# Kernel optimization log

Hardware: AMD Instinct MI355X
Metric: run time of the kernel (lower is better)

The kernel has to match this reference:

```python
import jax, jax.numpy as jnp
import numpy as np

N_NODES = 100000
D = 128
N_EDGES = 800000


def setup_inputs() -> dict:
    key = jax.random.key(0)
    k_feat, k_src, k_dst, k_ws, k_wn = jax.random.split(key, 5)
    scale = 1.0 / np.sqrt(D)
    return {
        "features": jax.random.normal(k_feat, (N_NODES, D), jnp.float32),
        "src": jax.random.randint(k_src, (N_EDGES,), 0, N_NODES, jnp.int32),
        "dst": jax.random.randint(k_dst, (N_EDGES,), 0, N_NODES, jnp.int32),
        "gamma": jnp.ones((D,), jnp.float32),
        "beta": jnp.zeros((D,), jnp.float32),
        "W_self": jax.random.normal(k_ws, (D, D), jnp.float32) * scale,
        "W_neigh": jax.random.normal(k_wn, (D, D), jnp.float32) * scale,
        "b": jnp.zeros((D,), jnp.float32),
    }


def reference(features, src, dst, gamma, beta, W_self, W_neigh, b):
    n = features.shape[0]
    eps = 1e-5
    # BatchNorm1d (training mode: batch stats over the node dim, biased var)
    mean = jnp.mean(features, axis=0)
    var = jnp.mean(jnp.square(features - mean), axis=0)
    h = (features - mean) * jax.lax.rsqrt(var + eps) * gamma + beta  # [N, D]

    # SAGEConv 'mean': gather source feats along edges, mean-reduce per dst node
    msg = h[src]  # [E, D] irregular gather
    agg = jax.ops.segment_sum(msg, dst, num_segments=n)  # [N, D]
    deg = jax.ops.segment_sum(jnp.ones(src.shape, h.dtype), dst, num_segments=n)
    h_neigh = agg / jnp.maximum(deg, 1.0)[:, None]  # zero-degree nodes stay 0

    conv = h @ W_self + h_neigh @ W_neigh + b  # fc_self + fc_neigh + bias
    out = conv + h  # skip connection
    return jax.nn.gelu(out, approximate=False)
```

## Files before the change

kernel.cpp:

```cpp
#include <hip/hip_runtime.h>

#define DD 128
#define NPB_LOG 8
#define NPB 256
#define EPB 2048

typedef __attribute__((ext_vector_type(8))) short short8;
typedef __attribute__((ext_vector_type(4))) float f32x4;
typedef __attribute__((ext_vector_type(2))) float f32x2;

__device__ inline unsigned short f2bf(float f) {
    unsigned u = __float_as_uint(f);
    unsigned r = u + 0x7fffu + ((u >> 16) & 1u);
    return (unsigned short)(r >> 16);
}

__global__ __launch_bounds__(256) void phase1_k(
    const float4* __restrict__ x, float* __restrict__ stats16, int n,
    const int* __restrict__ dst, int nE, int NCHUNK, int NBUCK,
    const float* __restrict__ Wself, const float* __restrict__ Wneigh,
    unsigned short* __restrict__ Bpre, int* __restrict__ cm) {
    int b = blockIdx.x, tid = threadIdx.x;
    __shared__ float ls[8][256];
    if (b < NCHUNK) {
        int chunk = b;
        int* cnt = (int*)ls;
        for (int i = tid; i < NBUCK; i += 256) cnt[i] = 0;
        __syncthreads();
        int e0 = chunk * EPB;
#pragma unroll
        for (int j = 0; j < 8; ++j) {
            int e = e0 + j * 256 + tid;
            if (e < nE) atomicAdd(&cnt[dst[e] >> NPB_LOG], 1);
        }
        __syncthreads();
        for (int bk = tid; bk < NBUCK; bk += 256)
            cm[(size_t)bk * NCHUNK + chunk] = cnt[bk];
    } else if (b < NCHUNK + 16) {
        int q = (b - NCHUNK) * 256 + tid;
        int l = q & 63;
        int kb = ((q >> 9) << 5) + ((l >> 4) << 3);
        int nn = (((q >> 6) & 7) << 4) + (l & 15);
        bool self = (kb < 128);
        const float* Wp = self ? (Wself + (size_t)kb * 128 + nn)
                               : (Wneigh + (size_t)(kb - 128) * 128 + nn);
        unsigned tmp[4];
#pragma unroll
        for (int j = 0; j < 4; ++j) {
            float v0 = Wp[(2 * j) * 128];
            float v1 = Wp[(2 * j + 1) * 128];
            if (self) {
                if (kb + 2 * j == nn) v0 += 1.0f;
                if (kb + 2 * j + 1 == nn) v1 += 1.0f;
            }
            tmp[j] = (unsigned)f2bf(v0) | ((unsigned)f2bf(v1) << 16);
        }
        uint4 w; w.x = tmp[0]; w.y = tmp[1]; w.z = tmp[2]; w.w = tmp[3];
        *(uint4*)(Bpre + (size_t)q * 8) = w;
    } else {
        int bb = b - NCHUNK - 16;
        int c4 = tid & 31, sub = tid >> 5;
        float sx = 0.f, sy = 0.f, sz = 0.f, sw = 0.f;
        float qx = 0.f, qy = 0.f, qz = 0.f, qw = 0.f;
        for (int r = bb * 8 + sub; r < n; r += 1024 * 8) {
            float4 v = x[(size_t)r * 32 + c4];
            sx += v.x; sy += v.y; sz += v.z; sw += v.w;
            qx += v.x * v.x; qy += v.y * v.y; qz += v.z * v.z; qw += v.w * v.w;
        }
        ls[sub][c4 * 4 + 0] = sx; ls[sub][c4 * 4 + 1] = sy;
        ls[sub][c4 * 4 + 2] = sz; ls[sub][c4 * 4 + 3] = sw;
        ls[sub][128 + c4 * 4 + 0] = qx; ls[sub][128 + c4 * 4 + 1] = qy;
        ls[sub][128 + c4 * 4 + 2] = qz; ls[sub][128 + c4 * 4 + 3] = qw;
        __syncthreads();
        float t = 0.f;
#pragma unroll
        for (int k = 0; k < 8; ++k) t += ls[k][tid];
        atomicAdd(&stats16[(bb & 15) * 256 + tid], t);
    }
}

__global__ __launch_bounds__(256) void scanA_k(
    const int* __restrict__ v_in, int* __restrict__ bsum, int n) {
    int b = blockIdx.x, t = threadIdx.x;
    int i0 = b * 1024 + t * 4;
    int4 v = {0, 0, 0, 0};
    if (i0 + 3 < n) v = *(const int4*)(v_in + i0);
    else {
        if (i0 < n) v.x = v_in[i0];
        if (i0 + 1 < n) v.y = v_in[i0 + 1];
        if (i0 + 2 < n) v.z = v_in[i0 + 2];
    }
    __shared__ int ls[256];
    ls[t] = v.x + v.y + v.z + v.w;
    __syncthreads();
#pragma unroll
    for (int off = 128; off > 0; off >>= 1) {
        if (t < off) ls[t] += ls[t + off];
        __syncthreads();
    }
    if (t == 0) bsum[b] = ls[0];
}

__global__ __launch_bounds__(256) void scanB_k(
    const int* __restrict__ bsum, int* __restrict__ bpref,
    int* __restrict__ total_out, int nb, int n,
    const float* __restrict__ stats16, const float* __restrict__ gamma,
    const float* __restrict__ beta, float* __restrict__ scsh, float inv_n) {
    int t = threadIdx.x;
    if (t < 128) {
        float s = 0.f, q = 0.f;
#pragma unroll
        for (int sh = 0; sh < 16; ++sh) {
            s += stats16[sh * 256 + t];
            q += stats16[sh * 256 + 128 + t];
        }
        float mean = s * inv_n;
        float var = q * inv_n - mean * mean;
        float sc = rsqrtf(var + 1e-5f) * gamma[t];
        scsh[t] = sc;
        scsh[128 + t] = beta[t] - mean * sc;
    }
    __shared__ int ls[256];
    ls[t] = (t < nb) ? bsum[t] : 0;
    __syncthreads();
#pragma unroll
    for (int off = 1; off < 256; off <<= 1) {
        int x = (t >= off) ? ls[t - off] : 0;
        __syncthreads();
        ls[t] += x;
        __syncthreads();
    }
    if (t < nb) bpref[t] = (t == 0) ? 0 : ls[t - 1];
    if (t == nb - 1) total_out[n] = ls[t];
}

__global__ __launch_bounds__(256) void scanC_k(
    const int* __restrict__ v_in, const int* __restrict__ bpref,
    int* __restrict__ o1, int* __restrict__ o2, int n) {
    int b = blockIdx.x, t = threadIdx.x;
    int i0 = b * 1024 + t * 4;
    int4 v = {0, 0, 0, 0};
    if (i0 + 3 < n) v = *(const int4*)(v_in + i0);
    else {
        if (i0 < n) v.x = v_in[i0];
        if (i0 + 1 < n) v.y = v_in[i0 + 1];
        if (i0 + 2 < n) v.z = v_in[i0 + 2];
    }
    int s = v.x + v.y + v.z + v.w;
    __shared__ int ls[256];
    ls[t] = s;
    __syncthreads();
#pragma unroll
    for (int off = 1; off < 256; off <<= 1) {
        int x = (t >= off) ? ls[t - off] : 0;
        __syncthreads();
        ls[t] += x;
        __syncthreads();
    }
    int run = bpref[b] + ((t == 0) ? 0 : ls[t - 1]);
    int4 o;
    o.x = run; o.y = run + v.x; o.z = o.y + v.y; o.w = o.z + v.z;
    if (i0 + 3 < n) {
        *(int4*)(o1 + i0) = o;
        *(int4*)(o2 + i0) = o;
    } else {
        if (i0 < n) { o1[i0] = o.x; o2[i0] = o.x; }
        if (i0 + 1 < n) { o1[i0 + 1] = o.y; o2[i0 + 1] = o.y; }
        if (i0 + 2 < n) { o1[i0 + 2] = o.z; o2[i0 + 2] = o.z; }
    }
}

__global__ __launch_bounds__(256) void phase2_k(
    const float4* __restrict__ x, const float* __restrict__ scsh,
    uint2* __restrict__ hbuf, unsigned* __restrict__ h8, int n,
    const int* __restrict__ src, const int* __restrict__ dst,
    const int* __restrict__ cmscan, unsigned* __restrict__ pairs,
    int nE, int NCHUNK, int NBUCK) {
    int b = blockIdx.x, tid = threadIdx.x;
    __shared__ int a[512];
    __shared__ int lcur[512];
    __shared__ int bas[512];
    __shared__ unsigned lsorted[EPB];
    __shared__ unsigned short lbk[EPB];
    if (b < NCHUNK) {
        int chunk = b;
        int e0 = chunk * EPB;
        int nv = min(EPB, nE - e0);
        for (int i = tid; i < 512; i += 256) a[i] = 0;
        __syncthreads();
        int myd[8];
#pragma unroll
        for (int j = 0; j < 8; ++j) {
            int e = e0 + j * 256 + tid;
            int d = (e < nE) ? dst[e] : -1;
            myd[j] = d;
            if (d >= 0) atomicAdd(&a[d >> NPB_LOG], 1);
        }
        for (int bk = tid; bk < NBUCK; bk += 256)
            bas[bk] = cmscan[(size_t)bk * NCHUNK + chunk];
        __syncthreads();
        for (int d = 1; d < 512; d <<= 1) {
            int idx = (tid + 1) * (d << 1) - 1;
            if (idx < 512) a[idx] += a[idx - d];
            __syncthreads();
        }
        if (tid == 0) a[511] = 0;
        __syncthreads();
        for (int d = 256; d >= 1; d >>= 1) {
            int idx = (tid + 1) * (d << 1) - 1;
            if (idx < 512) { int tm = a[idx - d]; a[idx - d] = a[idx]; a[idx] += tm; }
            __syncthreads();
        }
        for (int i = tid; i < 512; i += 256) lcur[i] = a[i];
        __syncthreads();
#pragma unroll
        for (int j = 0; j < 8; ++j) {
            int d = myd[j];
            if (d >= 0) {
                int e = e0 + j * 256 + tid;
                int bk = d >> NPB_LOG;
                int lp = atomicAdd(&lcur[bk], 1);
                lsorted[lp] = ((unsigned)src[e] << NPB_LOG) | (unsigned)(d & (NPB - 1));
                lbk[lp] = (unsigned short)bk;
            }
        }
        __syncthreads();
        for (int i = tid; i < nv; i += 256) {
            int bk = lbk[i];
            pairs[bas[bk] + i - a[bk]] = lsorted[i];
        }
    } else {
        int blk = b - NCHUNK;
        int c4 = tid & 31, sub = tid >> 5;
        int r0 = blk * 16 + sub, r1 = r0 + 8;
        float4 sc = ((const float4*)scsh)[c4];
        float4 sh = ((const float4*)(scsh + 128))[c4];
        bool ok0 = r0 < n, ok1 = r1 < n;
        float4 v0, v1;
        if (ok0) v0 = x[(size_t)r0 * 32 + c4];
        if (ok1) v1 = x[(size_t)r1 * 32 + c4];
        if (ok0) {
            float hx = v0.x * sc.x + sh.x, hy = v0.y * sc.y + sh.y;
            float hz = v0.z * sc.z + sh.z, hw = v0.w * sc.w + sh.w;
            uint2 o;
            o.x = (unsigned)f2bf(hx) | ((unsigned)f2bf(hy) << 16);
            o.y = (unsigned)f2bf(hz) | ((unsigned)f2bf(hw) << 16);
            hbuf[(size_t)r0 * 32 + c4] = o;
            int p8 = __builtin_amdgcn_cvt_pk_fp8_f32(hx, hy, 0, false);
            p8 = __builtin_amdgcn_cvt_pk_fp8_f32(hz, hw, p8, true);
            h8[(size_t)r0 * 32 + c4] = (unsigned)p8;
        }
        if (ok1) {
            float hx = v1.x * sc.x + sh.x, hy = v1.y * sc.y + sh.y;
            float hz = v1.z * sc.z + sh.z, hw = v1.w * sc.w + sh.w;
            uint2 o;
            o.x = (unsigned)f2bf(hx) | ((unsigned)f2bf(hy) << 16);
            o.y = (unsigned)f2bf(hz) | ((unsigned)f2bf(hw) << 16);
            hbuf[(size_t)r1 * 32 + c4] = o;
            int p8 = __builtin_amdgcn_cvt_pk_fp8_f32(hx, hy, 0, false);
            p8 = __builtin_amdgcn_cvt_pk_fp8_f32(hz, hw, p8, true);
            h8[(size_t)r1 * 32 + c4] = (unsigned)p8;
        }
    }
}

__global__ __launch_bounds__(256) void sortC_k(
    const unsigned* __restrict__ pairs, const int* __restrict__ cmscan,
    int* __restrict__ offsets, int* __restrict__ csr,
    int n, int nE, int NCHUNK, int NBUCK) {
    int b = blockIdx.x, tid = threadIdx.x;
    int base0 = cmscan[(size_t)b * NCHUNK];
    int end = (b + 1 < NBUCK) ? cmscan[(size_t)(b + 1) * NCHUNK] : nE;
    __shared__ int cnt[NPB];
    __shared__ int cur[NPB];
    cnt[tid] = 0;
    __syncthreads();
    for (int e = base0 + tid; e < end; e += 256)
        atomicAdd(&cnt[pairs[e] & (NPB - 1)], 1);
    __syncthreads();
    int c0 = cnt[tid];
    __shared__ int ps[256];
    ps[tid] = c0;
    __syncthreads();
#pragma unroll
    for (int off = 1; off < 256; off <<= 1) {
        int v = (tid >= off) ? ps[tid - off] : 0;
        __syncthreads();
        ps[tid] += v;
        __syncthreads();
    }
    int ex = base0 + ps[tid] - c0;
    cur[tid] = ex;
    int node = b * NPB + tid;
    if (node < n) offsets[node] = ex;
    if (b == NBUCK - 1 && tid == 0) offsets[n] = nE;
    __syncthreads();
    for (int e = base0 + tid; e < end; e += 256) {
        unsigned u = pairs[e];
        int p = atomicAdd(&cur[u & (NPB - 1)], 1);
        csr[p] = (int)(u >> NPB_LOG);
    }
}

#define ACC8(v)                                                       \
    do {                                                              \
        acc[0] += __builtin_amdgcn_cvt_pk_f32_fp8((v).x, false);      \
        acc[1] += __builtin_amdgcn_cvt_pk_f32_fp8((v).x, true);       \
        acc[2] += __builtin_amdgcn_cvt_pk_f32_fp8((v).y, false);      \
        acc[3] += __builtin_amdgcn_cvt_pk_f32_fp8((v).y, true);       \
        acc[4] += __builtin_amdgcn_cvt_pk_f32_fp8((v).z, false);      \
        acc[5] += __builtin_amdgcn_cvt_pk_f32_fp8((v).z, true);       \
        acc[6] += __builtin_amdgcn_cvt_pk_f32_fp8((v).w, false);      \
        acc[7] += __builtin_amdgcn_cvt_pk_f32_fp8((v).w, true);       \
    } while (0)

__global__ __launch_bounds__(256) void pull_k(
    const int* __restrict__ offsets, const int* __restrict__ csr,
    const uint4* __restrict__ h8q, uint4* __restrict__ hnw, int n) {
    int wv = (blockIdx.x * 256 + threadIdx.x) >> 6;
    int lane = threadIdx.x & 63;
    int g = lane >> 3, sl = lane & 7;
    int node = wv * 8 + g;
    bool valid = node < n;
    int nc = valid ? node : (n - 1);
    int b0 = offsets[nc], b1 = offsets[nc + 1];
    f32x2 acc[8];
#pragma unroll
    for (int k = 0; k < 8; ++k) acc[k] = f32x2{0.f, 0.f};
    int j = b0;
    for (; j + 4 <= b1; j += 4) {
        int i0 = csr[j], i1 = csr[j + 1], i2 = csr[j + 2], i3 = csr[j + 3];
        uint4 v0 = h8q[(size_t)i0 * 8 + sl];
        uint4 v1 = h8q[(size_t)i1 * 8 + sl];
        uint4 v2 = h8q[(size_t)i2 * 8 + sl];
        uint4 v3 = h8q[(size_t)i3 * 8 + sl];
        ACC8(v0); ACC8(v1); ACC8(v2); ACC8(v3);
    }
    if (j + 2 <= b1) {
        int i0 = csr[j], i1 = csr[j + 1];
        uint4 v0 = h8q[(size_t)i0 * 8 + sl];
        uint4 v1 = h8q[(size_t)i1 * 8 + sl];
        ACC8(v0); ACC8(v1);
        j += 2;
    }
    if (j < b1) {
        int i0 = csr[j];
        uint4 v0 = h8q[(size_t)i0 * 8 + sl];
        ACC8(v0);
    }
    if (valid) {
        float rd = (b1 > b0) ? 1.0f / (float)(b1 - b0) : 0.0f;
        unsigned ow[8];
#pragma unroll
        for (int k = 0; k < 8; ++k)
            ow[k] = (unsigned)f2bf(acc[k].x * rd) |
                    ((unsigned)f2bf(acc[k].y * rd) << 16);
        uint4 o1; o1.x = ow[0]; o1.y = ow[1]; o1.z = ow[2]; o1.w = ow[3];
        uint4 o2; o2.x = ow[4]; o2.y = ow[5]; o2.z = ow[6]; o2.w = ow[7];
        hnw[(size_t)node * 16 + sl * 2] = o1;
        hnw[(size_t)node * 16 + sl * 2 + 1] = o2;
    }
}

__global__ __launch_bounds__(256, 2) void gemm_k(
    const unsigned short* __restrict__ h, const unsigned short* __restrict__ hn,
    const unsigned short* __restrict__ Bpre, const float* __restrict__ bias,
    float* __restrict__ out, int n) {
    __shared__ unsigned short Bsw[32768];
    int tid = threadIdx.x, wave = tid >> 6, lane = tid & 63;
    int rb = blockIdx.x;
#pragma unroll
    for (int i = 0; i < 16; ++i) {
        int g = wave * 16 + i;
        __builtin_amdgcn_global_load_lds(
            (const __attribute__((address_space(1))) void*)(
                Bpre + ((size_t)g * 64 + lane) * 8),
            (__attribute__((address_space(3))) void*)(Bsw + (size_t)g * 512),
            16, 0, 0);
    }
    __syncthreads();

    int quad = lane >> 4, mrow = lane & 15;
    int r0 = rb * 128 + wave * 32;
    int rA0 = min(r0 + mrow, n - 1);
    int rA1 = min(r0 + 16 + mrow, n - 1);

    f32x4 zero = {0.0f, 0.0f, 0.0f, 0.0f};
    f32x4 acc[2][8];
#pragma unroll
    for (int m = 0; m < 2; ++m)
#pragma unroll
        for (int t = 0; t < 8; ++t) acc[m][t] = zero;

#pragma unroll
    for (int s = 0; s < 8; ++s) {
        int kb = s * 32 + quad * 8;
        short8 a0, a1;
        if (s < 4) {
            a0 = *(const short8*)(h + (size_t)rA0 * 128 + kb);
            a1 = *(const short8*)(h + (size_t)rA1 * 128 + kb);
        } else {
            int kk = kb - 128;
            a0 = *(const short8*)(hn + (size_t)rA0 * 128 + kk);
            a1 = *(const short8*)(hn + (size_t)rA1 * 128 + kk);
        }
#pragma unroll
        for (int tt = 0; tt < 8; ++tt) {
            short8 b = *(const short8*)(Bsw + ((size_t)(s * 8 + tt) * 64 + lane) * 8);
            acc[0][tt] = __builtin_amdgcn_mfma_f32_16x16x32_bf16(a0, b, acc[0][tt], 0, 0, 0);
            acc[1][tt] = __builtin_amdgcn_mfma_f32_16x16x32_bf16(a1, b, acc[1][tt], 0, 0, 0);
        }
    }

    float bi[8];
#pragma unroll
    for (int t = 0; t < 8; ++t) bi[t] = bias[t * 16 + mrow];
#pragma unroll
    for (int m = 0; m < 2; ++m) {
#pragma unroll
        for (int i = 0; i < 4; ++i) {
            int row = r0 + m * 16 + quad * 4 + i;
            if (row < n) {
#pragma unroll
                for (int t = 0; t < 8; ++t) {
                    int col = t * 16 + mrow;
                    float xv = acc[m][t][i] + bi[t];
                    float x2 = xv * xv;
                    float u = 0.7978845608f * xv * (1.0f + 0.044715f * x2);
                    float e = __expf(2.0f * u);
                    float th = 1.0f - 2.0f * __builtin_amdgcn_rcpf(e + 1.0f);
                    out[(size_t)row * 128 + col] = 0.5f * xv * (1.0f + th);
                }
            }
        }
    }
}

extern "C" void kernel_launch(void* const* d_in, const int* in_sizes, int n_in,
                              void* d_out, int out_size, void* d_ws, size_t ws_size,
                              hipStream_t stream) {
    const float* features = (const float*)d_in[0];
    const int* src = (const int*)d_in[1];
    const int* dst = (const int*)d_in[2];
    const float* gamma = (const float*)d_in[3];
    const float* beta = (const float*)d_in[4];
    const float* Wself = (const float*)d_in[5];
    const float* Wneigh = (const float*)d_in[6];
    const float* bias = (const float*)d_in[7];
    int n = in_sizes[0] / DD;
    int nE = in_sizes[1];
    int NCHUNK = (nE + EPB - 1) / EPB;
    int NBUCK = (n + NPB - 1) / NPB;
    int CM = NBUCK * NCHUNK;
    int tilesCM = (CM + 1023) / 1024;
    int nbNorm16 = (n + 15) / 16;

    auto align1k = [](size_t x) { return (x + 1023) & ~(size_t)1023; };
    char* ws = (char*)d_ws;
    size_t off = 0;
    float* stats16 = (float*)(ws + off);       off += 16384;
    float* scsh   = (float*)(ws + off);        off += 2048;
    int* cm       = (int*)(ws + off);          off += align1k((size_t)(CM + 1) * 4);
    int* cmscan   = (int*)(ws + off);          off += align1k((size_t)CM * 4);
    int* offsets  = (int*)(ws + off);          off += align1k((size_t)(n + 1) * 4);
    int* csr      = (int*)(ws + off);          off += align1k((size_t)nE * 4);
    unsigned* pairs = (unsigned*)(ws + off);   off += align1k((size_t)nE * 4);
    int* bsum     = (int*)(ws + off);          off += 1024;
    int* bpref    = (int*)(ws + off);          off += 1024;
    unsigned short* Bpre = (unsigned short*)(ws + off); off += 65536;
    unsigned short* hbuf = (unsigned short*)(ws + off); off += (size_t)n * 256;
    unsigned short* hnbuf = (unsigned short*)(ws + off); off += (size_t)n * 256;
    unsigned* h8 = (unsigned*)(ws + off);      off += (size_t)n * 128;

    hipMemsetAsync(stats16, 0, 16384, stream);

    phase1_k<<<NCHUNK + 16 + 1024, 256, 0, stream>>>(
        (const float4*)features, stats16, n, dst, nE, NCHUNK, NBUCK,
        Wself, Wneigh, Bpre, cm);
    scanA_k<<<tilesCM, 256, 0, stream>>>(cm, bsum, CM);
    scanB_k<<<1, 256, 0, stream>>>(bsum, bpref, cm, tilesCM, CM,
                                   stats16, gamma, beta, scsh, 1.0f / (float)n);
    scanC_k<<<tilesCM, 256, 0, stream>>>(cm, bpref, cmscan, cmscan, CM);
    phase2_k<<<NCHUNK + nbNorm16, 256, 0, stream>>>(
        (const float4*)features, scsh, (uint2*)hbuf, h8, n,
        src, dst, cmscan, pairs, nE, NCHUNK, NBUCK);
    sortC_k<<<NBUCK, 256, 0, stream>>>(pairs, cmscan, offsets, csr, n, nE,
                                       NCHUNK, NBUCK);
    {
        int waves = (n + 7) / 8;
        int blocks = (waves * 64 + 255) / 256;
        pull_k<<<blocks, 256, 0, stream>>>(
            offsets, csr, (const uint4*)h8, (uint4*)hnbuf, n);
    }
    gemm_k<<<(n + 127) / 128, 256, 0, stream>>>(
        hbuf, hnbuf, Bpre, bias, (float*)d_out, n);
}
```

Measured before the change: 192.4 us.

## Replace three-kernel scan with single-pass decoupled lookback scan; double edges per chunk

The scanA/scanB/scanC pipeline over the chunk-by-bucket count matrix is replaced by one kernel that publishes per-block aggregates and inclusive prefixes through atomic descriptors and spins on predecessors (decoupled lookback). This removes two kernel launches and the intermediate block-sum passes, at the cost of spin-waiting that relies on earlier blocks being scheduled. Separately, edges per chunk go from 2048 to 4096, which halves the number of chunks and the size of the count matrix, but adds per-thread registers and reduces parallelism in the bucketing kernels. The descriptor array is zeroed together with the stats buffer in the existing memset.

```diff
diff --git a/kernel.cpp b/kernel.cpp
--- a/kernel.cpp
+++ b/kernel.cpp
@@ -3,7 +3,8 @@
 #define DD 128
 #define NPB_LOG 8
 #define NPB 256
-#define EPB 2048
+#define EPB 4096
+#define EPT 16
 
 typedef __attribute__((ext_vector_type(8))) short short8;
 typedef __attribute__((ext_vector_type(4))) float f32x4;
@@ -29,7 +30,7 @@
         __syncthreads();
         int e0 = chunk * EPB;
 #pragma unroll
-        for (int j = 0; j < 8; ++j) {
+        for (int j = 0; j < EPT; ++j) {
             int e = e0 + j * 256 + tid;
             if (e < nE) atomicAdd(&cnt[dst[e] >> NPB_LOG], 1);
         }
@@ -79,35 +80,13 @@
     }
 }
 
-__global__ __launch_bounds__(256) void scanA_k(
-    const int* __restrict__ v_in, int* __restrict__ bsum, int n) {
-    int b = blockIdx.x, t = threadIdx.x;
-    int i0 = b * 1024 + t * 4;
-    int4 v = {0, 0, 0, 0};
-    if (i0 + 3 < n) v = *(const int4*)(v_in + i0);
-    else {
-        if (i0 < n) v.x = v_in[i0];
-        if (i0 + 1 < n) v.y = v_in[i0 + 1];
-        if (i0 + 2 < n) v.z = v_in[i0 + 2];
-    }
-    __shared__ int ls[256];
-    ls[t] = v.x + v.y + v.z + v.w;
-    __syncthreads();
-#pragma unroll
-    for (int off = 128; off > 0; off >>= 1) {
-        if (t < off) ls[t] += ls[t + off];
-        __syncthreads();
-    }
-    if (t == 0) bsum[b] = ls[0];
-}
-
-__global__ __launch_bounds__(256) void scanB_k(
-    const int* __restrict__ bsum, int* __restrict__ bpref,
-    int* __restrict__ total_out, int nb, int n,
+__global__ __launch_bounds__(256) void scanF_k(
+    const int* __restrict__ v_in, unsigned long long* __restrict__ desc,
+    int* __restrict__ out, int nCM,
     const float* __restrict__ stats16, const float* __restrict__ gamma,
     const float* __restrict__ beta, float* __restrict__ scsh, float inv_n) {
-    int t = threadIdx.x;
-    if (t < 128) {
+    int b = blockIdx.x, t = threadIdx.x;
+    if (b == 0 && t < 128) {
         float s = 0.f, q = 0.f;
 #pragma unroll
         for (int sh = 0; sh < 16; ++sh) {
@@ -120,8 +99,18 @@
         scsh[t] = sc;
         scsh[128 + t] = beta[t] - mean * sc;
     }
+    int i0 = b * 1024 + t * 4;
+    int4 v = {0, 0, 0, 0};
+    if (i0 + 3 < nCM) v = *(const int4*)(v_in + i0);
+    else {
+        if (i0 < nCM) v.x = v_in[i0];
+        if (i0 + 1 < nCM) v.y = v_in[i0 + 1];
+        if (i0 + 2 < nCM) v.z = v_in[i0 + 2];
+    }
+    int s4 = v.x + v.y + v.z + v.w;
     __shared__ int ls[256];
-    ls[t] = (t < nb) ? bsum[t] : 0;
+    __shared__ int sExcl;
+    ls[t] = s4;
     __syncthreads();
 #pragma unroll
     for (int off = 1; off < 256; off <<= 1) {
@@ -130,43 +119,35 @@
         ls[t] += x;
         __syncthreads();
     }
-    if (t < nb) bpref[t] = (t == 0) ? 0 : ls[t - 1];
-    if (t == nb - 1) total_out[n] = ls[t];
-}
-
-__global__ __launch_bounds__(256) void scanC_k(
-    const int* __restrict__ v_in, const int* __restrict__ bpref,
-    int* __restrict__ o1, int* __restrict__ o2, int n) {
-    int b = blockIdx.x, t = threadIdx.x;
-    int i0 = b * 1024 + t * 4;
-    int4 v = {0, 0, 0, 0};
-    if (i0 + 3 < n) v = *(const int4*)(v_in + i0);
-    else {
-        if (i0 < n) v.x = v_in[i0];
-        if (i0 + 1 < n) v.y = v_in[i0 + 1];
-        if (i0 + 2 < n) v.z = v_in[i0 + 2];
-    }
-    int s = v.x + v.y + v.z + v.w;
-    __shared__ int ls[256];
-    ls[t] = s;
-    __syncthreads();
-#pragma unroll
-    for (int off = 1; off < 256; off <<= 1) {
-        int x = (t >= off) ? ls[t - off] : 0;
-        __syncthreads();
-        ls[t] += x;
-        __syncthreads();
-    }
-    int run = bpref[b] + ((t == 0) ? 0 : ls[t - 1]);
+    if (t == 0) {
+        int blockTotal = ls[255];
+        __hip_atomic_store(&desc[b], (1ull << 32) | (unsigned)blockTotal,
+                           __ATOMIC_RELEASE, __HIP_MEMORY_SCOPE_AGENT);
+        int excl = 0;
+        for (int i = b - 1; i >= 0;) {
+            unsigned long long d;
+            do {
+                d = __hip_atomic_load(&desc[i], __ATOMIC_ACQUIRE,
+                                      __HIP_MEMORY_SCOPE_AGENT);
+            } while ((d >> 32) == 0ull);
+            excl += (int)(unsigned)d;
+            if ((d >> 32) == 2ull) break;
+            --i;
+        }
+        __hip_atomic_store(&desc[b],
+                           (2ull << 32) | (unsigned)(excl + blockTotal),
+                           __ATOMIC_RELEASE, __HIP_MEMORY_SCOPE_AGENT);
+        sExcl = excl;
+    }
+    __syncthreads();
+    int run = sExcl + ((t == 0) ? 0 : ls[t - 1]);
     int4 o;
     o.x = run; o.y = run + v.x; o.z = o.y + v.y; o.w = o.z + v.z;
-    if (i0 + 3 < n) {
-        *(int4*)(o1 + i0) = o;
-        *(int4*)(o2 + i0) = o;
-    } else {
-        if (i0 < n) { o1[i0] = o.x; o2[i0] = o.x; }
-        if (i0 + 1 < n) { o1[i0 + 1] = o.y; o2[i0 + 1] = o.y; }
-        if (i0 + 2 < n) { o1[i0 + 2] = o.z; o2[i0 + 2] = o.z; }
+    if (i0 + 3 < nCM) *(int4*)(out + i0) = o;
+    else {
+        if (i0 < nCM) out[i0] = o.x;
+        if (i0 + 1 < nCM) out[i0 + 1] = o.y;
+        if (i0 + 2 < nCM) out[i0 + 2] = o.z;
     }
 }
 
@@ -188,9 +169,9 @@
         int nv = min(EPB, nE - e0);
         for (int i = tid; i < 512; i += 256) a[i] = 0;
         __syncthreads();
-        int myd[8];
-#pragma unroll
-        for (int j = 0; j < 8; ++j) {
+        int myd[EPT];
+#pragma unroll
+        for (int j = 0; j < EPT; ++j) {
             int e = e0 + j * 256 + tid;
             int d = (e < nE) ? dst[e] : -1;
             myd[j] = d;
@@ -214,7 +195,7 @@
         for (int i = tid; i < 512; i += 256) lcur[i] = a[i];
         __syncthreads();
 #pragma unroll
-        for (int j = 0; j < 8; ++j) {
+        for (int j = 0; j < EPT; ++j) {
             int d = myd[j];
             if (d >= 0) {
                 int e = e0 + j * 256 + tid;
@@ -459,28 +440,27 @@
     char* ws = (char*)d_ws;
     size_t off = 0;
     float* stats16 = (float*)(ws + off);       off += 16384;
+    unsigned long long* desc = (unsigned long long*)(ws + off); off += 1024;
+    size_t zeroBytes = off;
     float* scsh   = (float*)(ws + off);        off += 2048;
-    int* cm       = (int*)(ws + off);          off += align1k((size_t)(CM + 1) * 4);
+    int* cm       = (int*)(ws + off);          off += align1k((size_t)CM * 4);
     int* cmscan   = (int*)(ws + off);          off += align1k((size_t)CM * 4);
     int* offsets  = (int*)(ws + off);          off += align1k((size_t)(n + 1) * 4);
     int* csr      = (int*)(ws + off);          off += align1k((size_t)nE * 4);
     unsigned* pairs = (unsigned*)(ws + off);   off += align1k((size_t)nE * 4);
-    int* bsum     = (int*)(ws + off);          off += 1024;
-    int* bpref    = (int*)(ws + off);          off += 1024;
     unsigned short* Bpre = (unsigned short*)(ws + off); off += 65536;
     unsigned short* hbuf = (unsigned short*)(ws + off); off += (size_t)n * 256;
     unsigned short* hnbuf = (unsigned short*)(ws + off); off += (size_t)n * 256;
     unsigned* h8 = (unsigned*)(ws + off);      off += (size_t)n * 128;
 
-    hipMemsetAsync(stats16, 0, 16384, stream);
+    hipMemsetAsync(stats16, 0, zeroBytes, stream);
 
     phase1_k<<<NCHUNK + 16 + 1024, 256, 0, stream>>>(
         (const float4*)features, stats16, n, dst, nE, NCHUNK, NBUCK,
         Wself, Wneigh, Bpre, cm);
-    scanA_k<<<tilesCM, 256, 0, stream>>>(cm, bsum, CM);
-    scanB_k<<<1, 256, 0, stream>>>(bsum, bpref, cm, tilesCM, CM,
-                                   stats16, gamma, beta, scsh, 1.0f / (float)n);
-    scanC_k<<<tilesCM, 256, 0, stream>>>(cm, bpref, cmscan, cmscan, CM);
+    scanF_k<<<tilesCM, 256, 0, stream>>>(cm, desc, cmscan, CM,
+                                         stats16, gamma, beta, scsh,
+                                         1.0f / (float)n);
     phase2_k<<<NCHUNK + nbNorm16, 256, 0, stream>>>(
         (const float4*)features, scsh, (uint2*)hbuf, h8, n,
         src, dst, cmscan, pairs, nE, NCHUNK, NBUCK);
```

Result: slower. 203.1 us (+5.6%).
